# Kernel tuning notes

Hardware: AMD Instinct MI355X
Metric: run time of the kernel (lower is better)

## Reference

```python
import jax, jax.numpy as jnp
import numpy as np

GOP = 4


def conv3x3(x, w, b):
    y = jax.lax.conv_general_dilated(x, w, (1, 1), 'SAME',
                                     dimension_numbers=('NCHW', 'OIHW', 'NCHW'))
    return y + b[None, :, None, None]


def resize_bilinear(x, oh, ow):
    # F.interpolate(mode='bilinear', align_corners=False), no antialias
    N, C, H, W = x.shape
    ys = (jnp.arange(oh, dtype=x.dtype) + 0.5) * (H / oh) - 0.5
    xs = (jnp.arange(ow, dtype=x.dtype) + 0.5) * (W / ow) - 0.5
    y0 = jnp.floor(ys); x0 = jnp.floor(xs)
    ty = (ys - y0)[:, None]; tx = (xs - x0)[None, :]
    y0i = jnp.clip(y0, 0, H - 1).astype(jnp.int32)
    y1i = jnp.clip(y0 + 1, 0, H - 1).astype(jnp.int32)
    x0i = jnp.clip(x0, 0, W - 1).astype(jnp.int32)
    x1i = jnp.clip(x0 + 1, 0, W - 1).astype(jnp.int32)
    r00 = x[:, :, y0i][:, :, :, x0i]; r01 = x[:, :, y0i][:, :, :, x1i]
    r10 = x[:, :, y1i][:, :, :, x0i]; r11 = x[:, :, y1i][:, :, :, x1i]
    top = r00 * (1 - tx) + r01 * tx
    bot = r10 * (1 - tx) + r11 * tx
    return top * (1 - ty) + bot * ty


def deform_sample_1x1(feat, off):
    # torchvision deform_conv2d with 1x1 kernel: bilinear gather at
    # (h + dy, w + dx), zero outside; offset channels are (dy, dx).
    N, C, H, W = feat.shape
    dy, dx = off[:, 0], off[:, 1]                       # [N,H,W]
    gy = jnp.arange(H, dtype=feat.dtype)[:, None] + dy  # [N,H,W]
    gx = jnp.arange(W, dtype=feat.dtype)[None, :] + dx
    y0 = jnp.floor(gy); x0 = jnp.floor(gx)
    ty = (gy - y0)[:, None]; tx = (gx - x0)[:, None]    # [N,1,H,W]

    def corner(yi, xi):
        valid = (yi >= 0) & (yi < H) & (xi >= 0) & (xi < W)
        yc = jnp.clip(yi, 0, H - 1).astype(jnp.int32)
        xc = jnp.clip(xi, 0, W - 1).astype(jnp.int32)
        v = jax.vmap(lambda f, y, x: f[:, y, x])(feat, yc, xc)  # [N,C,H,W]
        return v * valid[:, None].astype(feat.dtype)

    return (corner(y0, x0) * (1 - ty) * (1 - tx)
            + corner(y0, x0 + 1) * (1 - ty) * tx
            + corner(y0 + 1, x0) * ty * (1 - tx)
            + corner(y0 + 1, x0 + 1) * ty * tx)


def setup_inputs() -> dict:
    key = jax.random.key(0)
    ks = jax.random.split(key, 20)
    dim = 256
    f32 = jnp.float32

    def p(k, shape, s=0.05):
        return jax.random.normal(k, shape, dtype=f32) * s

    return {
        'imgs': jax.random.normal(ks[0], (2, 16, 3, 224, 224), dtype=f32),
        'i_features': jax.random.normal(ks[1], (8, dim, 56, 56), dtype=f32),
        'p_motions': jax.random.normal(ks[2], (2, 12, 2, 112, 112), dtype=f32),
        'dw': p(ks[3], (dim, dim)), 'db': p(ks[4], (dim,)),
        'mw1': p(ks[5], (dim, dim, 3, 3)), 'mb1': p(ks[6], (dim,)),
        'mw2': p(ks[7], (dim, dim, 3, 3)), 'mb2': p(ks[8], (dim,)),
        'mw3': p(ks[9], (dim, dim, 3, 3)), 'mb3': p(ks[10], (dim,)),
        'ew1': p(ks[11], (dim, 2, 3, 3)), 'eb1': p(ks[12], (dim,)),
        'ew2': p(ks[13], (dim, dim, 3, 3)), 'eb2': p(ks[14], (dim,)),
        'ew3': p(ks[15], (dim, dim, 3, 3)), 'eb3': p(ks[16], (dim,)),
        'ew4': p(ks[17], (dim, dim, 3, 3)), 'eb4': p(ks[18], (dim,)),
    }


def reference(imgs, i_features, p_motions, dw, db, mw1, mb1, mw2, mb2, mw3, mb3,
              ew1, eb1, ew2, eb2, ew3, eb3, ew4, eb4):
    B = imgs.shape[0]
    num_gop = imgs.shape[1] // GOP
    h, w = i_features.shape[-2], i_features.shape[-1]
    scale = h / imgs.shape[-1]  # static python float
    Tp = p_motions.shape[1]
    k = Tp // num_gop

    # flatten motions over (b t), resize to feature res, rescale magnitudes
    pm = p_motions.reshape(B * Tp, 2, p_motions.shape[-2], p_motions.shape[-1])
    pm = resize_bilinear(pm, h, w) * scale              # [(b n k), 2, h, w]

    emb = jax.nn.relu(conv3x3(pm, ew1, eb1))
    emb = jax.nn.relu(conv3x3(emb, ew2, eb2))
    emb = jax.nn.relu(conv3x3(emb, ew3, eb3))
    emb = jax.nn.relu(conv3x3(emb, ew4, eb4))

    # i_features expanded to one copy per P-frame: (b n) -> (b n k)
    feat = jnp.repeat(i_features, k, axis=0)
    sampled = deform_sample_1x1(feat, pm)
    pf = jnp.einsum('nchw,oc->nohw', sampled, dw) + db[None, :, None, None]

    pf = jax.nn.relu(conv3x3(pf, mw1, mb1))
    pf = jax.nn.relu(conv3x3(pf, mw2, mb2))
    pf = jax.nn.relu(conv3x3(pf, mw3, mb3))
    p2d = pf + emb                                      # [(b n k), c, h, w]

    # adaptive_avg_pool2d(1) + flatten(3)
    pooled = p2d.reshape(B, num_gop, k, -1, h, w).mean(axis=(-2, -1))  # [b,n,k,c]
    return pooled, p2d
```

## Files before the change

kernel.cpp:

```cpp
#include <hip/hip_runtime.h>

#define NPIX 3136
#define NN   24
#define CDIM 256

typedef __attribute__((ext_vector_type(8))) short short8v;
typedef __attribute__((ext_vector_type(4))) float float4v;

typedef __attribute__((address_space(1))) const void gvoid;
typedef __attribute__((address_space(3))) void lvoid;
static __device__ __forceinline__ void async_copy16(const void* g, void* l) {
    __builtin_amdgcn_global_load_lds((gvoid*)g, (lvoid*)l, 16, 0, 0);
}

static __device__ __forceinline__ unsigned short f2b(float f) {
    unsigned int u = __float_as_uint(f);
    u = (u + 0x7FFFu + ((u >> 16) & 1u)) >> 16;
    return (unsigned short)u;
}
static __device__ __forceinline__ float b2f(unsigned short h) {
    return __uint_as_float(((unsigned int)h) << 16);
}

__global__ __launch_bounds__(256) void resize_pm_kernel(
    const float* __restrict__ pmo, float* __restrict__ pm)
{
    int idx = blockIdx.x * 256 + threadIdx.x;
    if (idx >= NN * 2 * NPIX) return;
    int x = idx % 56, y = (idx / 56) % 56, nc = idx / NPIX;
    const float* src = pmo + (size_t)nc * 112 * 112 + (size_t)(2 * y) * 112 + 2 * x;
    pm[idx] = (src[0] + src[1] + src[112] + src[113]) * 0.0625f;
}

__global__ __launch_bounds__(256) void pack_all_kernel(
    const float* __restrict__ s0, const float* __restrict__ s1,
    const float* __restrict__ s2, const float* __restrict__ s3,
    const float* __restrict__ s4, const float* __restrict__ s5,
    const float* __restrict__ sdw, unsigned short* __restrict__ dstbase)
{
    int bx = blockIdx.x;
    if (bx < 6 * 2304) {
        int wi = bx / 2304;
        int d = (bx % 2304) * 256 + threadIdx.x;
        const float* w = (wi == 0) ? s0 : (wi == 1) ? s1 : (wi == 2) ? s2
                       : (wi == 3) ? s3 : (wi == 4) ? s4 : s5;
        int j = d & 7;
        int lane = (d >> 3) & 63;
        int g = (d >> 9) & 3;
        int e = d >> 11;
        int tap = e % 9;
        int f = e / 9;
        int ch = f & 7, cb = f >> 3;
        int co = cb * 64 + g * 16 + (lane & 15);
        int ci = ch * 32 + (lane >> 4) * 8 + j;
        dstbase[(size_t)wi * 589824 + d] = f2b(w[((size_t)co * 256 + ci) * 9 + tap]);
    } else {
        int d = (bx - 6 * 2304) * 256 + threadIdx.x;
        int j = d & 7;
        int lane = (d >> 3) & 63;
        int g = (d >> 9) & 3;
        int ch = (d >> 11) & 7;
        int cb = d >> 14;
        int co = cb * 64 + g * 16 + (lane & 15);
        int ci = ch * 32 + (lane >> 4) * 8 + j;
        dstbase[(size_t)6 * 589824 + d] = f2b(sdw[(size_t)co * 256 + ci]);
    }
}

__global__ __launch_bounds__(256) void ew1_kernel(
    const float* __restrict__ pm, const float* __restrict__ w,
    const float* __restrict__ b, unsigned short* __restrict__ out)
{
    __shared__ float sT[8][18];
    __shared__ float sW1[256 * 19];
    int n = blockIdx.y;
    int pixbase = blockIdx.x * 8;
    int t = threadIdx.x;
    if (t < 144) {
        int p = t / 18, j = t % 18;
        int ci = j / 9, tap = j % 9;
        int pix = pixbase + p;
        int y = pix / 56, x = pix % 56;
        int yy = y + tap / 3 - 1, xx = x + tap % 3 - 1;
        float v = 0.f;
        if ((unsigned)yy < 56u && (unsigned)xx < 56u)
            v = pm[((size_t)n * 2 + ci) * NPIX + yy * 56 + xx];
        sT[p][j] = v;
    }
    for (int idx = t; idx < 4608; idx += 256) {
        int co = idx / 18, j = idx % 18;
        sW1[co * 19 + j] = w[idx];
    }
    __syncthreads();
    int co = t;
    float bias = b[co];
#pragma unroll
    for (int p = 0; p < 8; p++) {
        float acc = bias;
#pragma unroll
        for (int j = 0; j < 18; j++) acc += sT[p][j] * sW1[co * 19 + j];
        acc = fmaxf(acc, 0.f);
        out[((size_t)n * NPIX + pixbase + p) * 256 + co] = f2b(acc);
    }
}

template <int TAPS, bool RELU, bool HASB, bool FUSE>
__global__ __launch_bounds__(256, 2) void conv_mfma(
    const unsigned short* __restrict__ in,
    const unsigned short* __restrict__ wp,
    const float* __restrict__ bias,
    unsigned short* __restrict__ out,
    const unsigned short* __restrict__ inB,
    const unsigned short* __restrict__ wpB,
    const float* __restrict__ biasB,
    unsigned short* __restrict__ outB,
    int zsplit,
    const unsigned short* __restrict__ emb,
    float* __restrict__ dout)
{
    constexpr int W_ITERS = TAPS * 4;
    constexpr int SIN_SHORTS = (TAPS == 9) ? 10 * 58 * 32 : 448 * 32;

    __shared__ unsigned short sIn[SIN_SHORTS];
    __shared__ unsigned short sW[W_ITERS * 512];

    const int r0 = blockIdx.x * 8;
    if (r0 >= 56) return;
    const int tid = threadIdx.x;
    const int lane = tid & 63;
    const int wv = tid >> 6;
    const int col = lane & 15;
    const int quad = lane >> 4;
    const int cb = blockIdx.y;

    int n = blockIdx.z;
    const unsigned short* inP = in;
    const unsigned short* wpP = wp;
    const float* biasP = bias;
    unsigned short* outP = out;
    if (n >= zsplit) {
        n -= zsplit;
        inP = inB; wpP = wpB; biasP = biasB; outP = outB;
    }

    const unsigned short* inN = inP + (size_t)n * NPIX * 256;
    const unsigned short* wcb = wpP + (size_t)cb * 8 * W_ITERS * 512;

    int rowoff[7];
#pragma unroll
    for (int nj = 0; nj < 7; nj++) {
        int pxl = wv * 112 + nj * 16 + col;
        if (TAPS == 9) {
            int yl = pxl / 56;
            rowoff[nj] = yl * 58 + (pxl - yl * 56);
        } else {
            rowoff[nj] = pxl;
        }
    }
    const int qoff = quad * 8;
    const int laneSrc = (lane >> 2) * 256 + (lane & 3) * 8;

    if (TAPS == 9) {
        for (int i = tid * 8; i < SIN_SHORTS; i += 2048)
            *(int4*)(sIn + i) = (int4){0, 0, 0, 0};
    }

    float4v acc[4][7];
#pragma unroll
    for (int mi = 0; mi < 4; mi++)
#pragma unroll
        for (int nj = 0; nj < 7; nj++) acc[mi][nj] = (float4v){0.f, 0.f, 0.f, 0.f};

    for (int ch = 0; ch < 8; ch++) {
        const int c0 = ch * 32;
        __syncthreads();
        const unsigned short* wchunk = wcb + (size_t)ch * W_ITERS * 512;
#pragma unroll
        for (int it = wv; it < W_ITERS; it += 4)
            async_copy16(wchunk + it * 512 + lane * 8, sW + it * 512);
        if (TAPS == 9) {
#pragma unroll
            for (int ry = 0; ry < 10; ry++) {
                int k = (wv - ry) & 3;
                int gy = r0 + ry - 1;
                if ((unsigned)gy < 56u && (k < 3 || lane < 32))
                    async_copy16(inN + (size_t)gy * 14336 + k * 4096 + c0 + laneSrc,
                                 sIn + ry * 1856 + 32 + k * 512);
            }
        } else {
#pragma unroll
            for (int k = 0; k < 7; k++) {
                int it = wv + k * 4;
                async_copy16(inN + (size_t)r0 * 14336 + it * 4096 + c0 + laneSrc,
                             sIn + it * 512);
            }
        }
        __syncthreads();
#pragma unroll
        for (int tap = 0; tap < TAPS; tap++) {
            const int coff = (TAPS == 9) ? ((tap / 3) * 58 + (tap % 3)) * 32 : 0;
            short8v a[4], b[7];
#pragma unroll
            for (int mi = 0; mi < 4; mi++)
                a[mi] = *(const short8v*)(sW + ((tap * 4 + mi) * 64 + lane) * 8);
#pragma unroll
            for (int nj = 0; nj < 7; nj++)
                b[nj] = *(const short8v*)(sIn + rowoff[nj] * 32 + coff + qoff);
#pragma unroll
            for (int mi = 0; mi < 4; mi++)
#pragma unroll
                for (int nj = 0; nj < 7; nj++)
                    acc[mi][nj] = __builtin_amdgcn_mfma_f32_16x16x32_bf16(
                        a[mi], b[nj], acc[mi][nj], 0, 0, 0);
        }
    }

    if (!FUSE) {
        unsigned short* outT = outP + ((size_t)n * NPIX + r0 * 56 + wv * 112) * 256 + cb * 64;
#pragma unroll
        for (int mi = 0; mi < 4; mi++) {
            float4v bv = (float4v){0.f, 0.f, 0.f, 0.f};
            if (HASB) bv = *(const float4v*)(biasP + cb * 64 + mi * 16 + quad * 4);
#pragma unroll
            for (int nj = 0; nj < 7; nj++) {
                float v0 = acc[mi][nj][0] + bv[0];
                float v1 = acc[mi][nj][1] + bv[1];
                float v2 = acc[mi][nj][2] + bv[2];
                float v3 = acc[mi][nj][3] + bv[3];
                if (RELU) {
                    v0 = fmaxf(v0, 0.f); v1 = fmaxf(v1, 0.f);
                    v2 = fmaxf(v2, 0.f); v3 = fmaxf(v3, 0.f);
                }
                uint2 pk;
                pk.x = (unsigned)f2b(v0) | ((unsigned)f2b(v1) << 16);
                pk.y = (unsigned)f2b(v2) | ((unsigned)f2b(v3) << 16);
                *(uint2*)(outT + ((size_t)(nj * 16 + col)) * 256 + mi * 16 + quad * 4) = pk;
            }
        }
    } else {
        const int pixBase = r0 * 56 + wv * 112;
        float* p2d = dout + 6144 + (size_t)n * CDIM * NPIX;
        float sums[4][4];
#pragma unroll
        for (int mi = 0; mi < 4; mi++)
#pragma unroll
            for (int q = 0; q < 4; q++) sums[mi][q] = 0.f;
#pragma unroll
        for (int mi = 0; mi < 4; mi++) {
            float4v bv = *(const float4v*)(biasP + cb * 64 + mi * 16 + quad * 4);
            const int co0 = cb * 64 + mi * 16 + quad * 4;
#pragma unroll
            for (int nj = 0; nj < 7; nj++) {
                int pix = pixBase + nj * 16 + col;
                uint2 e = *(const uint2*)(emb + ((size_t)n * NPIX + pix) * 256 + co0);
                float v0 = fmaxf(acc[mi][nj][0] + bv[0], 0.f) + b2f((unsigned short)(e.x & 0xFFFF));
                float v1 = fmaxf(acc[mi][nj][1] + bv[1], 0.f) + b2f((unsigned short)(e.x >> 16));
                float v2 = fmaxf(acc[mi][nj][2] + bv[2], 0.f) + b2f((unsigned short)(e.y & 0xFFFF));
                float v3 = fmaxf(acc[mi][nj][3] + bv[3], 0.f) + b2f((unsigned short)(e.y >> 16));
                p2d[(size_t)(co0 + 0) * NPIX + pix] = v0;
                p2d[(size_t)(co0 + 1) * NPIX + pix] = v1;
                p2d[(size_t)(co0 + 2) * NPIX + pix] = v2;
                p2d[(size_t)(co0 + 3) * NPIX + pix] = v3;
                sums[mi][0] += v0; sums[mi][1] += v1;
                sums[mi][2] += v2; sums[mi][3] += v3;
            }
        }
#pragma unroll
        for (int mi = 0; mi < 4; mi++)
#pragma unroll
            for (int q = 0; q < 4; q++) {
                float s = sums[mi][q];
                s += __shfl_down(s, 8, 16);
                s += __shfl_down(s, 4, 16);
                s += __shfl_down(s, 2, 16);
                s += __shfl_down(s, 1, 16);
                if (col == 0)
                    atomicAdd(dout + n * CDIM + cb * 64 + mi * 16 + quad * 4 + q,
                              s * (1.f / 3136.f));
            }
    }
}

__global__ __launch_bounds__(256) void transpose_fI(
    const float* __restrict__ feat, unsigned short* __restrict__ dst)
{
    __shared__ float s[64][65];
    int fi = blockIdx.z;
    int p0 = blockIdx.x * 64;
    int c0 = blockIdx.y * 64;
    int t = threadIdx.x;
    int pl = t & 63, cq = t >> 6;
#pragma unroll
    for (int i = 0; i < 16; i++) {
        int c = cq + i * 4;
        s[pl][c] = feat[((size_t)fi * 256 + c0 + c) * NPIX + p0 + pl];
    }
    __syncthreads();
    int cl = t & 63, pq = t >> 6;
#pragma unroll
    for (int i = 0; i < 16; i++) {
        int p = pq + i * 4;
        dst[((size_t)fi * NPIX + p0 + p) * 256 + c0 + cl] = f2b(s[p][cl]);
    }
}

__global__ __launch_bounds__(256) void deform_kernel(
    const unsigned short* __restrict__ Z,
    const float* __restrict__ pm,
    const float* __restrict__ db,
    unsigned short* __restrict__ out)
{
    int n = blockIdx.y;
    int t = threadIdx.x;
    int pix = blockIdx.x * 8 + (t >> 5);
    int g = t & 31;
    int fi = n / 3;
    int y = pix / 56, x = pix % 56;
    float dy = pm[((size_t)n * 2 + 0) * NPIX + pix];
    float dx = pm[((size_t)n * 2 + 1) * NPIX + pix];
    float gy = (float)y + dy, gx = (float)x + dx;
    float y0f = floorf(gy), x0f = floorf(gx);
    float ty = gy - y0f, tx = gx - x0f;
    int y0 = (int)y0f, x0 = (int)x0f, y1 = y0 + 1, x1 = x0 + 1;
    bool vy0 = (unsigned)y0 < 56u, vy1 = (unsigned)y1 < 56u;
    bool vx0 = (unsigned)x0 < 56u, vx1 = (unsigned)x1 < 56u;
    float w00 = (1.f - ty) * (1.f - tx) * (vy0 && vx0 ? 1.f : 0.f);
    float w01 = (1.f - ty) * tx * (vy0 && vx1 ? 1.f : 0.f);
    float w10 = ty * (1.f - tx) * (vy1 && vx0 ? 1.f : 0.f);
    float w11 = ty * tx * (vy1 && vx1 ? 1.f : 0.f);
    int y0c = vy0 ? y0 : 0, y1c = vy1 ? y1 : 0;
    int x0c = vx0 ? x0 : 0, x1c = vx1 ? x1 : 0;
    const unsigned short* Zf = Z + (size_t)fi * NPIX * 256 + g * 8;
    const unsigned short* p00 = Zf + (size_t)(y0c * 56 + x0c) * 256;
    const unsigned short* p01 = Zf + (size_t)(y0c * 56 + x1c) * 256;
    const unsigned short* p10 = Zf + (size_t)(y1c * 56 + x0c) * 256;
    const unsigned short* p11 = Zf + (size_t)(y1c * 56 + x1c) * 256;
    unsigned short r[8];
#pragma unroll
    for (int j = 0; j < 8; j++) {
        float v = b2f(p00[j]) * w00 + b2f(p01[j]) * w01 +
                  b2f(p10[j]) * w10 + b2f(p11[j]) * w11;
        v += db[g * 8 + j];
        r[j] = f2b(v);
    }
    *(int4*)(out + ((size_t)n * NPIX + pix) * 256 + g * 8) = *(int4*)r;
}

extern "C" void kernel_launch(void* const* d_in, const int* in_sizes, int n_in,
                              void* d_out, int out_size, void* d_ws, size_t ws_size,
                              hipStream_t stream)
{
    const float* i_features = (const float*)d_in[1];
    const float* p_motions  = (const float*)d_in[2];
    const float* dw  = (const float*)d_in[3];
    const float* db  = (const float*)d_in[4];
    const float* mw1 = (const float*)d_in[5];
    const float* mb1 = (const float*)d_in[6];
    const float* mw2 = (const float*)d_in[7];
    const float* mb2 = (const float*)d_in[8];
    const float* mw3 = (const float*)d_in[9];
    const float* mb3 = (const float*)d_in[10];
    const float* ew1 = (const float*)d_in[11];
    const float* eb1 = (const float*)d_in[12];
    const float* ew2 = (const float*)d_in[13];
    const float* eb2 = (const float*)d_in[14];
    const float* ew3 = (const float*)d_in[15];
    const float* eb3 = (const float*)d_in[16];
    const float* ew4 = (const float*)d_in[17];
    const float* eb4 = (const float*)d_in[18];
    float* out = (float*)d_out;

    const size_t SZ_PM  = 602112;
    const size_t SZ_WPK = 7208960;
    const size_t SZ_ACT = 38535168;
    char* p = (char*)d_ws;
    float* pm = (float*)p;            p += SZ_PM;
    unsigned short* wpk = (unsigned short*)p;
    unsigned short* wpE2 = wpk + 0 * 589824;
    unsigned short* wpE3 = wpk + 1 * 589824;
    unsigned short* wpE4 = wpk + 2 * 589824;
    unsigned short* wpM1 = wpk + 3 * 589824;
    unsigned short* wpM2 = wpk + 4 * 589824;
    unsigned short* wpM3 = wpk + 5 * 589824;
    unsigned short* wpDW = wpk + 6 * 589824;
    p += SZ_WPK;
    unsigned short* bufA = (unsigned short*)p; p += SZ_ACT;
    unsigned short* bufB = (unsigned short*)p; p += SZ_ACT;
    unsigned short* bufC = (unsigned short*)p; p += SZ_ACT;
    unsigned short* bufD = (unsigned short*)p;

    const bool paired = ws_size >= SZ_PM + SZ_WPK + 4 * SZ_ACT;

    hipMemsetAsync(out, 0, 6144 * sizeof(float), stream);

    resize_pm_kernel<<<(NN * 2 * NPIX + 255) / 256, 256, 0, stream>>>(p_motions, pm);
    pack_all_kernel<<<6 * 2304 + 256, 256, 0, stream>>>(
        ew2, ew3, ew4, mw1, mw2, mw3, dw, wpk);

    dim3 cg24(8, 4, NN), cg48(8, 4, 2 * NN), cg8(8, 4, 8);

    if (paired) {
        ew1_kernel<<<dim3(392, NN), 256, 0, stream>>>(pm, ew1, eb1, bufA);
        conv_mfma<9, true, true, false><<<cg24, 256, 0, stream>>>(
            bufA, wpE2, eb2, bufB,  bufA, wpE2, eb2, bufB, NN, nullptr, nullptr);
        unsigned short* fI = bufA;
        unsigned short* Zb = bufA + (size_t)8 * NPIX * 256;
        transpose_fI<<<dim3(49, 4, 8), 256, 0, stream>>>(i_features, fI);
        conv_mfma<1, false, false, false><<<cg8, 256, 0, stream>>>(
            fI, wpDW, nullptr, Zb,  fI, wpDW, nullptr, Zb, NN, nullptr, nullptr);
        deform_kernel<<<dim3(392, NN), 256, 0, stream>>>(Zb, pm, db, bufC);
        conv_mfma<9, true, true, false><<<cg48, 256, 0, stream>>>(
            bufB, wpE3, eb3, bufA,  bufC, wpM1, mb1, bufD, NN, nullptr, nullptr);
        conv_mfma<9, true, true, false><<<cg48, 256, 0, stream>>>(
            bufA, wpE4, eb4, bufB,  bufD, wpM2, mb2, bufC, NN, nullptr, nullptr);
        conv_mfma<9, true, true, true><<<cg24, 256, 0, stream>>>(
            bufC, wpM3, mb3, nullptr,  bufC, wpM3, mb3, nullptr, NN, bufB, out);
    } else {
        ew1_kernel<<<dim3(392, NN), 256, 0, stream>>>(pm, ew1, eb1, bufA);
        conv_mfma<9, true, true, false><<<cg24, 256, 0, stream>>>(
            bufA, wpE2, eb2, bufB,  bufA, wpE2, eb2, bufB, NN, nullptr, nullptr);
        conv_mfma<9, true, true, false><<<cg24, 256, 0, stream>>>(
            bufB, wpE3, eb3, bufA,  bufB, wpE3, eb3, bufA, NN, nullptr, nullptr);
        conv_mfma<9, true, true, false><<<cg24, 256, 0, stream>>>(
            bufA, wpE4, eb4, bufC,  bufA, wpE4, eb4, bufC, NN, nullptr, nullptr);
        transpose_fI<<<dim3(49, 4, 8), 256, 0, stream>>>(i_features, bufA);
        conv_mfma<1, false, false, false><<<cg8, 256, 0, stream>>>(
            bufA, wpDW, nullptr, bufB,  bufA, wpDW, nullptr, bufB, NN, nullptr, nullptr);
        deform_kernel<<<dim3(392, NN), 256, 0, stream>>>(bufB, pm, db, bufA);
        conv_mfma<9, true, true, false><<<cg24, 256, 0, stream>>>(
            bufA, wpM1, mb1, bufB,  bufA, wpM1, mb1, bufB, NN, nullptr, nullptr);
        conv_mfma<9, true, true, false><<<cg24, 256, 0, stream>>>(
            bufB, wpM2, mb2, bufA,  bufB, wpM2, mb2, bufA, NN, nullptr, nullptr);
        conv_mfma<9, true, true, true><<<cg24, 256, 0, stream>>>(
            bufA, wpM3, mb3, nullptr,  bufA, wpM3, mb3, nullptr, NN, bufC, out);
    }
}
```

Before: 692.3 us.

## Double-buffer LDS weight and input tiles in the MFMA conv kernel

Doubles the shared-memory buffers for weights and input tiles so the async global-to-LDS copies for the next 32-channel chunk are issued before computing the current chunk. This removes one barrier per chunk and is meant to hide global load latency behind the MFMA work. The cost is double the LDS footprint (roughly 148KB for the 3x3 variant), which likely drops occupancy from two blocks per CU to one. That could offset the gain from overlap.

```diff
diff --git a/kernel.cpp b/kernel.cpp
--- a/kernel.cpp
+++ b/kernel.cpp
@@ -120,9 +120,10 @@
 {
     constexpr int W_ITERS = TAPS * 4;
     constexpr int SIN_SHORTS = (TAPS == 9) ? 10 * 58 * 32 : 448 * 32;
-
-    __shared__ unsigned short sIn[SIN_SHORTS];
-    __shared__ unsigned short sW[W_ITERS * 512];
+    constexpr int SW_SHORTS = W_ITERS * 512;
+
+    __shared__ unsigned short sIn[2 * SIN_SHORTS];
+    __shared__ unsigned short sW[2 * SW_SHORTS];
 
     const int r0 = blockIdx.x * 8;
     if (r0 >= 56) return;
@@ -160,24 +161,16 @@
     const int qoff = quad * 8;
     const int laneSrc = (lane >> 2) * 256 + (lane & 3) * 8;
 
-    if (TAPS == 9) {
-        for (int i = tid * 8; i < SIN_SHORTS; i += 2048)
-            *(int4*)(sIn + i) = (int4){0, 0, 0, 0};
-    }
-
-    float4v acc[4][7];
-#pragma unroll
-    for (int mi = 0; mi < 4; mi++)
-#pragma unroll
-        for (int nj = 0; nj < 7; nj++) acc[mi][nj] = (float4v){0.f, 0.f, 0.f, 0.f};
-
-    for (int ch = 0; ch < 8; ch++) {
+    auto stageW = [&](int ch, int half) {
+        const unsigned short* wchunk = wcb + (size_t)ch * W_ITERS * 512;
+        unsigned short* dst = sW + half * SW_SHORTS;
+#pragma unroll
+        for (int it = wv; it < W_ITERS; it += 4)
+            async_copy16(wchunk + it * 512 + lane * 8, dst + it * 512);
+    };
+    auto stageI = [&](int ch, int half) {
         const int c0 = ch * 32;
-        __syncthreads();
-        const unsigned short* wchunk = wcb + (size_t)ch * W_ITERS * 512;
-#pragma unroll
-        for (int it = wv; it < W_ITERS; it += 4)
-            async_copy16(wchunk + it * 512 + lane * 8, sW + it * 512);
+        unsigned short* dst = sIn + half * SIN_SHORTS;
         if (TAPS == 9) {
 #pragma unroll
             for (int ry = 0; ry < 10; ry++) {
@@ -185,27 +178,51 @@
                 int gy = r0 + ry - 1;
                 if ((unsigned)gy < 56u && (k < 3 || lane < 32))
                     async_copy16(inN + (size_t)gy * 14336 + k * 4096 + c0 + laneSrc,
-                                 sIn + ry * 1856 + 32 + k * 512);
+                                 dst + ry * 1856 + 32 + k * 512);
             }
         } else {
 #pragma unroll
             for (int k = 0; k < 7; k++) {
                 int it = wv + k * 4;
                 async_copy16(inN + (size_t)r0 * 14336 + it * 4096 + c0 + laneSrc,
-                             sIn + it * 512);
+                             dst + it * 512);
             }
         }
+    };
+
+    if (TAPS == 9) {
+        for (int i = tid * 8; i < 2 * SIN_SHORTS; i += 2048)
+            *(int4*)(sIn + i) = (int4){0, 0, 0, 0};
         __syncthreads();
+    }
+
+    float4v acc[4][7];
+#pragma unroll
+    for (int mi = 0; mi < 4; mi++)
+#pragma unroll
+        for (int nj = 0; nj < 7; nj++) acc[mi][nj] = (float4v){0.f, 0.f, 0.f, 0.f};
+
+    stageW(0, 0);
+    stageI(0, 0);
+
+    for (int ch = 0; ch < 8; ch++) {
+        __syncthreads();
+        if (ch < 7) {
+            stageW(ch + 1, (ch + 1) & 1);
+            stageI(ch + 1, (ch + 1) & 1);
+        }
+        const int wOff = (ch & 1) * SW_SHORTS;
+        const int iOff = (ch & 1) * SIN_SHORTS;
 #pragma unroll
         for (int tap = 0; tap < TAPS; tap++) {
             const int coff = (TAPS == 9) ? ((tap / 3) * 58 + (tap % 3)) * 32 : 0;
             short8v a[4], b[7];
 #pragma unroll
             for (int mi = 0; mi < 4; mi++)
-                a[mi] = *(const short8v*)(sW + ((tap * 4 + mi) * 64 + lane) * 8);
+                a[mi] = *(const short8v*)(sW + wOff + ((tap * 4 + mi) * 64 + lane) * 8);
 #pragma unroll
             for (int nj = 0; nj < 7; nj++)
-                b[nj] = *(const short8v*)(sIn + rowoff[nj] * 32 + coff + qoff);
+                b[nj] = *(const short8v*)(sIn + iOff + rowoff[nj] * 32 + coff + qoff);
 #pragma unroll
             for (int mi = 0; mi < 4; mi++)
 #pragma unroll
```

Result: slower. 822.1 us (+18.8%).

## Add 512-thread conv kernel computing 128 output channels per block

Applied to the files above, without the earlier changes.

Adds a new conv8_mfma kernel in which each 512-thread block computes 128 output channels (two wave groups of 64) over 8 rows, instead of 64 channels with 256 threads. The weight packing layout is changed to match for all weights except the final fused conv, which keeps the old kernel and layout. The intent is to reuse each staged input tile across twice as many output channels, halving input LDS staging traffic per MFMA. In exchange the grid has half as many blocks and each block uses more LDS and registers, which may lower occupancy.

```diff
diff --git a/kernel.cpp b/kernel.cpp
--- a/kernel.cpp
+++ b/kernel.cpp
@@ -46,22 +46,33 @@
                        : (wi == 3) ? s3 : (wi == 4) ? s4 : s5;
         int j = d & 7;
         int lane = (d >> 3) & 63;
-        int g = (d >> 9) & 3;
-        int e = d >> 11;
-        int tap = e % 9;
-        int f = e / 9;
-        int ch = f & 7, cb = f >> 3;
-        int co = cb * 64 + g * 16 + (lane & 15);
-        int ci = ch * 32 + (lane >> 4) * 8 + j;
+        int co, ci, tap;
+        if (wi == 5) {
+            int g = (d >> 9) & 3;
+            int e = d >> 11;
+            tap = e % 9;
+            int f = e / 9;
+            int ch = f & 7, cb = f >> 3;
+            co = cb * 64 + g * 16 + (lane & 15);
+            ci = ch * 32 + (lane >> 4) * 8 + j;
+        } else {
+            int mi = (d >> 9) & 7;
+            int e = d >> 12;
+            tap = e % 9;
+            int f = e / 9;
+            int ch = f & 7, cb = f >> 3;
+            co = cb * 128 + mi * 16 + (lane & 15);
+            ci = ch * 32 + (lane >> 4) * 8 + j;
+        }
         dstbase[(size_t)wi * 589824 + d] = f2b(w[((size_t)co * 256 + ci) * 9 + tap]);
     } else {
         int d = (bx - 6 * 2304) * 256 + threadIdx.x;
         int j = d & 7;
         int lane = (d >> 3) & 63;
-        int g = (d >> 9) & 3;
-        int ch = (d >> 11) & 7;
-        int cb = d >> 14;
-        int co = cb * 64 + g * 16 + (lane & 15);
+        int mi = (d >> 9) & 7;
+        int e = d >> 12;
+        int ch = e & 7, cb = e >> 3;
+        int co = cb * 128 + mi * 16 + (lane & 15);
         int ci = ch * 32 + (lane >> 4) * 8 + j;
         dstbase[(size_t)6 * 589824 + d] = f2b(sdw[(size_t)co * 256 + ci]);
     }
@@ -101,6 +112,154 @@
         for (int j = 0; j < 18; j++) acc += sT[p][j] * sW1[co * 19 + j];
         acc = fmaxf(acc, 0.f);
         out[((size_t)n * NPIX + pixbase + p) * 256 + co] = f2b(acc);
+    }
+}
+
+template <int TAPS, bool RELU, bool HASB>
+__global__ __launch_bounds__(512, 2) void conv8_mfma(
+    const unsigned short* __restrict__ in,
+    const unsigned short* __restrict__ wp,
+    const float* __restrict__ bias,
+    unsigned short* __restrict__ out,
+    const unsigned short* __restrict__ inB,
+    const unsigned short* __restrict__ wpB,
+    const float* __restrict__ biasB,
+    unsigned short* __restrict__ outB,
+    int zsplit)
+{
+    constexpr int W_ITERS = TAPS * 8;
+    constexpr int SIN_SHORTS = (TAPS == 9) ? 10 * 58 * 32 : 448 * 32;
+
+    __shared__ unsigned short sIn[2 * SIN_SHORTS];
+    __shared__ unsigned short sW[W_ITERS * 512];
+
+    const int r0 = blockIdx.x * 8;
+    if (r0 >= 56) return;
+    const int tid = threadIdx.x;
+    const int lane = tid & 63;
+    const int wv = tid >> 6;
+    const int mih = wv >> 2;
+    const int wpx = wv & 3;
+    const int col = lane & 15;
+    const int quad = lane >> 4;
+    const int cb = blockIdx.y;
+
+    int n = blockIdx.z;
+    const unsigned short* inP = in;
+    const unsigned short* wpP = wp;
+    const float* biasP = bias;
+    unsigned short* outP = out;
+    if (n >= zsplit) {
+        n -= zsplit;
+        inP = inB; wpP = wpB; biasP = biasB; outP = outB;
+    }
+
+    const unsigned short* inN = inP + (size_t)n * NPIX * 256;
+    const unsigned short* wcb = wpP + (size_t)cb * 8 * W_ITERS * 512;
+
+    int rowoff[7];
+#pragma unroll
+    for (int nj = 0; nj < 7; nj++) {
+        int pxl = wpx * 112 + nj * 16 + col;
+        if (TAPS == 9) {
+            int yl = pxl / 56;
+            rowoff[nj] = yl * 58 + (pxl - yl * 56);
+        } else {
+            rowoff[nj] = pxl;
+        }
+    }
+    const int qoff = quad * 8;
+    const int laneSrc = (lane >> 2) * 256 + (lane & 3) * 8;
+
+    auto stageW = [&](int ch) {
+        const unsigned short* wchunk = wcb + (size_t)ch * W_ITERS * 512;
+#pragma unroll
+        for (int it = wv; it < W_ITERS; it += 8)
+            async_copy16(wchunk + it * 512 + lane * 8, sW + it * 512);
+    };
+    auto stageI = [&](int ch, int half) {
+        const int c0 = ch * 32;
+        unsigned short* dst = sIn + half * SIN_SHORTS;
+        if (TAPS == 9) {
+#pragma unroll
+            for (int s = wv; s < 40; s += 8) {
+                int ry = s >> 2, k = s & 3;
+                int gy = r0 + ry - 1;
+                if ((unsigned)gy < 56u && (k < 3 || lane < 32))
+                    async_copy16(inN + (size_t)gy * 14336 + k * 4096 + c0 + laneSrc,
+                                 dst + ry * 1856 + 32 + k * 512);
+            }
+        } else {
+#pragma unroll
+            for (int s = wv; s < 28; s += 8)
+                async_copy16(inN + (size_t)r0 * 14336 + s * 4096 + c0 + laneSrc,
+                             dst + s * 512);
+        }
+    };
+
+    if (TAPS == 9) {
+        for (int i = tid * 8; i < 2 * SIN_SHORTS; i += 512 * 8)
+            *(int4*)(sIn + i) = (int4){0, 0, 0, 0};
+        __syncthreads();
+    }
+
+    float4v acc[4][7];
+#pragma unroll
+    for (int mi = 0; mi < 4; mi++)
+#pragma unroll
+        for (int nj = 0; nj < 7; nj++) acc[mi][nj] = (float4v){0.f, 0.f, 0.f, 0.f};
+
+    stageW(0);
+    stageI(0, 0);
+
+    for (int ch = 0; ch < 8; ch++) {
+        __syncthreads();
+        if (ch < 7) stageI(ch + 1, (ch + 1) & 1);
+        const int iOff = (ch & 1) * SIN_SHORTS;
+#pragma unroll
+        for (int tap = 0; tap < TAPS; tap++) {
+            const int coff = (TAPS == 9) ? ((tap / 3) * 58 + (tap % 3)) * 32 : 0;
+            short8v a[4], b[7];
+#pragma unroll
+            for (int mi = 0; mi < 4; mi++)
+                a[mi] = *(const short8v*)(sW + ((tap * 8 + mih * 4 + mi) * 64 + lane) * 8);
+#pragma unroll
+            for (int nj = 0; nj < 7; nj++)
+                b[nj] = *(const short8v*)(sIn + iOff + rowoff[nj] * 32 + coff + qoff);
+#pragma unroll
+            for (int mi = 0; mi < 4; mi++)
+#pragma unroll
+                for (int nj = 0; nj < 7; nj++)
+                    acc[mi][nj] = __builtin_amdgcn_mfma_f32_16x16x32_bf16(
+                        a[mi], b[nj], acc[mi][nj], 0, 0, 0);
+        }
+        if (ch < 7) {
+            __syncthreads();
+            stageW(ch + 1);
+        }
+    }
+
+    unsigned short* outT = outP + ((size_t)n * NPIX + r0 * 56 + wpx * 112) * 256
+                         + cb * 128 + mih * 64;
+#pragma unroll
+    for (int mi = 0; mi < 4; mi++) {
+        float4v bv = (float4v){0.f, 0.f, 0.f, 0.f};
+        if (HASB) bv = *(const float4v*)(biasP + cb * 128 + mih * 64 + mi * 16 + quad * 4);
+#pragma unroll
+        for (int nj = 0; nj < 7; nj++) {
+            float v0 = acc[mi][nj][0] + bv[0];
+            float v1 = acc[mi][nj][1] + bv[1];
+            float v2 = acc[mi][nj][2] + bv[2];
+            float v3 = acc[mi][nj][3] + bv[3];
+            if (RELU) {
+                v0 = fmaxf(v0, 0.f); v1 = fmaxf(v1, 0.f);
+                v2 = fmaxf(v2, 0.f); v3 = fmaxf(v3, 0.f);
+            }
+            uint2 pk;
+            pk.x = (unsigned)f2b(v0) | ((unsigned)f2b(v1) << 16);
+            pk.y = (unsigned)f2b(v2) | ((unsigned)f2b(v3) << 16);
+            *(uint2*)(outT + ((size_t)(nj * 16 + col)) * 256 + mi * 16 + quad * 4) = pk;
+        }
     }
 }
 
@@ -397,41 +556,42 @@
     pack_all_kernel<<<6 * 2304 + 256, 256, 0, stream>>>(
         ew2, ew3, ew4, mw1, mw2, mw3, dw, wpk);
 
-    dim3 cg24(8, 4, NN), cg48(8, 4, 2 * NN), cg8(8, 4, 8);
+    dim3 cg24(8, 2, NN), cg48(8, 2, 2 * NN), cg8(8, 2, 8);
+    dim3 cgF(8, 4, NN);
 
     if (paired) {
         ew1_kernel<<<dim3(392, NN), 256, 0, stream>>>(pm, ew1, eb1, bufA);
-        conv_mfma<9, true, true, false><<<cg24, 256, 0, stream>>>(
-            bufA, wpE2, eb2, bufB,  bufA, wpE2, eb2, bufB, NN, nullptr, nullptr);
+        conv8_mfma<9, true, true><<<cg24, 512, 0, stream>>>(
+            bufA, wpE2, eb2, bufB,  bufA, wpE2, eb2, bufB, NN);
         unsigned short* fI = bufA;
         unsigned short* Zb = bufA + (size_t)8 * NPIX * 256;
         transpose_fI<<<dim3(49, 4, 8), 256, 0, stream>>>(i_features, fI);
-        conv_mfma<1, false, false, false><<<cg8, 256, 0, stream>>>(
-            fI, wpDW, nullptr, Zb,  fI, wpDW, nullptr, Zb, NN, nullptr, nullptr);
+        conv8_mfma<1, false, false><<<cg8, 512, 0, stream>>>(
+            fI, wpDW, nullptr, Zb,  fI, wpDW, nullptr, Zb, NN);
         deform_kernel<<<dim3(392, NN), 256, 0, stream>>>(Zb, pm, db, bufC);
-        conv_mfma<9, true, true, false><<<cg48, 256, 0, stream>>>(
-            bufB, wpE3, eb3, bufA,  bufC, wpM1, mb1, bufD, NN, nullptr, nullptr);
-        conv_mfma<9, true, true, false><<<cg48, 256, 0, stream>>>(
-            bufA, wpE4, eb4, bufB,  bufD, wpM2, mb2, bufC, NN, nullptr, nullptr);
-        conv_mfma<9, true, true, true><<<cg24, 256, 0, stream>>>(
+        conv8_mfma<9, true, true><<<cg48, 512, 0, stream>>>(
+            bufB, wpE3, eb3, bufA,  bufC, wpM1, mb1, bufD, NN);
+        conv8_mfma<9, true, true><<<cg48, 512, 0, stream>>>(
+            bufA, wpE4, eb4, bufB,  bufD, wpM2, mb2, bufC, NN);
+        conv_mfma<9, true, true, true><<<cgF, 256, 0, stream>>>(
             bufC, wpM3, mb3, nullptr,  bufC, wpM3, mb3, nullptr, NN, bufB, out);
     } else {
         ew1_kernel<<<dim3(392, NN), 256, 0, stream>>>(pm, ew1, eb1, bufA);
-        conv_mfma<9, true, true, false><<<cg24, 256, 0, stream>>>(
-            bufA, wpE2, eb2, bufB,  bufA, wpE2, eb2, bufB, NN, nullptr, nullptr);
-        conv_mfma<9, true, true, false><<<cg24, 256, 0, stream>>>(
-            bufB, wpE3, eb3, bufA,  bufB, wpE3, eb3, bufA, NN, nullptr, nullptr);
-        conv_mfma<9, true, true, false><<<cg24, 256, 0, stream>>>(
-            bufA, wpE4, eb4, bufC,  bufA, wpE4, eb4, bufC, NN, nullptr, nullptr);
+        conv8_mfma<9, true, true><<<cg24, 512, 0, stream>>>(
+            bufA, wpE2, eb2, bufB,  bufA, wpE2, eb2, bufB, NN);
+        conv8_mfma<9, true, true><<<cg24, 512, 0, stream>>>(
+            bufB, wpE3, eb3, bufA,  bufB, wpE3, eb3, bufA, NN);
+        conv8_mfma<9, true, true><<<cg24, 512, 0, stream>>>(
+            bufA, wpE4, eb4, bufC,  bufA, wpE4, eb4, bufC, NN);
         transpose_fI<<<dim3(49, 4, 8), 256, 0, stream>>>(i_features, bufA);
-        conv_mfma<1, false, false, false><<<cg8, 256, 0, stream>>>(
-            bufA, wpDW, nullptr, bufB,  bufA, wpDW, nullptr, bufB, NN, nullptr, nullptr);
+        conv8_mfma<1, false, false><<<cg8, 512, 0, stream>>>(
+            bufA, wpDW, nullptr, bufB,  bufA, wpDW, nullptr, bufB, NN);
         deform_kernel<<<dim3(392, NN), 256, 0, stream>>>(bufB, pm, db, bufA);
-        conv_mfma<9, true, true, false><<<cg24, 256, 0, stream>>>(
-            bufA, wpM1, mb1, bufB,  bufA, wpM1, mb1, bufB, NN, nullptr, nullptr);
-        conv_mfma<9, true, true, false><<<cg24, 256, 0, stream>>>(
-            bufB, wpM2, mb2, bufA,  bufB, wpM2, mb2, bufA, NN, nullptr, nullptr);
-        conv_mfma<9, true, true, true><<<cg24, 256, 0, stream>>>(
+        conv8_mfma<9, true, true><<<cg24, 512, 0, stream>>>(
+            bufA, wpM1, mb1, bufB,  bufA, wpM1, mb1, bufB, NN);
+        conv8_mfma<9, true, true><<<cg24, 512, 0, stream>>>(
+            bufB, wpM2, mb2, bufA,  bufB, wpM2, mb2, bufA, NN);
+        conv_mfma<9, true, true, true><<<cgF, 256, 0, stream>>>(
             bufA, wpM3, mb3, nullptr,  bufA, wpM3, mb3, nullptr, NN, bufC, out);
     }
 }
```

New measurement: 751.6 us. +8.6%, slower.

## Merge ew1 with fI transpose and pair conv2 with 1x1 projection in one launch

Applied to the files above, without the earlier changes.

Folds the i_features transpose into the ew1 kernel as extra blocks, and runs the first embedding 3x3 conv together with the 1x1 deform projection in a single heterogeneous launch via a templated conv_pair wrapper. The goal is fewer kernel launches and better GPU fill, since the small transpose and 1x1 conv grids used to run alone. To avoid aliasing, the fI/Zb scratch moves to bufD. In exchange, shared memory is sized for the 3x3 case in every variant, and the ew1 kernel now declares a large transpose tile it mostly leaves unused, which may reduce occupancy.

```diff
diff --git a/kernel.cpp b/kernel.cpp
--- a/kernel.cpp
+++ b/kernel.cpp
@@ -67,81 +67,87 @@
     }
 }
 
-__global__ __launch_bounds__(256) void ew1_kernel(
+__global__ __launch_bounds__(256) void ew1_fI_kernel(
     const float* __restrict__ pm, const float* __restrict__ w,
-    const float* __restrict__ b, unsigned short* __restrict__ out)
+    const float* __restrict__ b, unsigned short* __restrict__ outEw,
+    const float* __restrict__ feat, unsigned short* __restrict__ outFI,
+    int ewBlocks)
 {
     __shared__ float sT[8][18];
     __shared__ float sW1[256 * 19];
-    int n = blockIdx.y;
-    int pixbase = blockIdx.x * 8;
+    __shared__ float sTr[64][65];
+    int bx = blockIdx.x;
     int t = threadIdx.x;
-    if (t < 144) {
-        int p = t / 18, j = t % 18;
-        int ci = j / 9, tap = j % 9;
-        int pix = pixbase + p;
-        int y = pix / 56, x = pix % 56;
-        int yy = y + tap / 3 - 1, xx = x + tap % 3 - 1;
-        float v = 0.f;
-        if ((unsigned)yy < 56u && (unsigned)xx < 56u)
-            v = pm[((size_t)n * 2 + ci) * NPIX + yy * 56 + xx];
-        sT[p][j] = v;
-    }
-    for (int idx = t; idx < 4608; idx += 256) {
-        int co = idx / 18, j = idx % 18;
-        sW1[co * 19 + j] = w[idx];
-    }
-    __syncthreads();
-    int co = t;
-    float bias = b[co];
-#pragma unroll
-    for (int p = 0; p < 8; p++) {
-        float acc = bias;
-#pragma unroll
-        for (int j = 0; j < 18; j++) acc += sT[p][j] * sW1[co * 19 + j];
-        acc = fmaxf(acc, 0.f);
-        out[((size_t)n * NPIX + pixbase + p) * 256 + co] = f2b(acc);
+    if (bx < ewBlocks) {
+        int n = bx / 392;
+        int pixbase = (bx % 392) * 8;
+        if (t < 144) {
+            int p = t / 18, j = t % 18;
+            int ci = j / 9, tap = j % 9;
+            int pix = pixbase + p;
+            int y = pix / 56, x = pix % 56;
+            int yy = y + tap / 3 - 1, xx = x + tap % 3 - 1;
+            float v = 0.f;
+            if ((unsigned)yy < 56u && (unsigned)xx < 56u)
+                v = pm[((size_t)n * 2 + ci) * NPIX + yy * 56 + xx];
+            sT[p][j] = v;
+        }
+        for (int idx = t; idx < 4608; idx += 256) {
+            int co = idx / 18, j = idx % 18;
+            sW1[co * 19 + j] = w[idx];
+        }
+        __syncthreads();
+        int co = t;
+        float bias = b[co];
+#pragma unroll
+        for (int p = 0; p < 8; p++) {
+            float acc = bias;
+#pragma unroll
+            for (int j = 0; j < 18; j++) acc += sT[p][j] * sW1[co * 19 + j];
+            acc = fmaxf(acc, 0.f);
+            outEw[((size_t)n * NPIX + pixbase + p) * 256 + co] = f2b(acc);
+        }
+    } else {
+        int b2 = bx - ewBlocks;
+        int fi = b2 / 196;
+        int rem = b2 % 196;
+        int c0 = (rem / 49) * 64;
+        int p0 = (rem % 49) * 64;
+        int pl = t & 63, cq = t >> 6;
+#pragma unroll
+        for (int i = 0; i < 16; i++) {
+            int c = cq + i * 4;
+            sTr[pl][c] = feat[((size_t)fi * 256 + c0 + c) * NPIX + p0 + pl];
+        }
+        __syncthreads();
+        int cl = t & 63, pq = t >> 6;
+#pragma unroll
+        for (int i = 0; i < 16; i++) {
+            int p = pq + i * 4;
+            outFI[((size_t)fi * NPIX + p0 + p) * 256 + c0 + cl] = f2b(sTr[p][cl]);
+        }
     }
 }
 
 template <int TAPS, bool RELU, bool HASB, bool FUSE>
-__global__ __launch_bounds__(256, 2) void conv_mfma(
-    const unsigned short* __restrict__ in,
-    const unsigned short* __restrict__ wp,
-    const float* __restrict__ bias,
-    unsigned short* __restrict__ out,
-    const unsigned short* __restrict__ inB,
-    const unsigned short* __restrict__ wpB,
-    const float* __restrict__ biasB,
-    unsigned short* __restrict__ outB,
-    int zsplit,
+static __device__ __forceinline__ void conv_body(
+    unsigned short* sIn, unsigned short* sW,
+    const unsigned short* __restrict__ inP,
+    const unsigned short* __restrict__ wpP,
+    const float* __restrict__ biasP,
+    unsigned short* __restrict__ outP,
+    int n, int r0, int cb,
     const unsigned short* __restrict__ emb,
     float* __restrict__ dout)
 {
     constexpr int W_ITERS = TAPS * 4;
     constexpr int SIN_SHORTS = (TAPS == 9) ? 10 * 58 * 32 : 448 * 32;
 
-    __shared__ unsigned short sIn[SIN_SHORTS];
-    __shared__ unsigned short sW[W_ITERS * 512];
-
-    const int r0 = blockIdx.x * 8;
-    if (r0 >= 56) return;
     const int tid = threadIdx.x;
     const int lane = tid & 63;
     const int wv = tid >> 6;
     const int col = lane & 15;
     const int quad = lane >> 4;
-    const int cb = blockIdx.y;
-
-    int n = blockIdx.z;
-    const unsigned short* inP = in;
-    const unsigned short* wpP = wp;
-    const float* biasP = bias;
-    unsigned short* outP = out;
-    if (n >= zsplit) {
-        n -= zsplit;
-        inP = inB; wpP = wpB; biasP = biasB; outP = outB;
-    }
 
     const unsigned short* inN = inP + (size_t)n * NPIX * 256;
     const unsigned short* wcb = wpP + (size_t)cb * 8 * W_ITERS * 512;
@@ -279,6 +285,32 @@
                               s * (1.f / 3136.f));
             }
     }
+}
+
+template <int TA, bool RA, bool HA, int TB, bool RB, bool HB, bool FUSE>
+__global__ __launch_bounds__(256, 2) void conv_pair(
+    const unsigned short* __restrict__ inA,
+    const unsigned short* __restrict__ wpA,
+    const float* __restrict__ bA, unsigned short* __restrict__ oA,
+    const unsigned short* __restrict__ inB,
+    const unsigned short* __restrict__ wpB,
+    const float* __restrict__ bB, unsigned short* __restrict__ oB,
+    int zsplit,
+    const unsigned short* __restrict__ emb,
+    float* __restrict__ dout)
+{
+    __shared__ unsigned short sIn[10 * 58 * 32];
+    __shared__ unsigned short sW[36 * 512];
+
+    const int r0 = blockIdx.x * 8;
+    if (r0 >= 56) return;
+    int n = blockIdx.z;
+    if (n >= zsplit)
+        conv_body<TB, RB, HB, FUSE>(sIn, sW, inB, wpB, bB, oB,
+                                    n - zsplit, r0, blockIdx.y, emb, dout);
+    else
+        conv_body<TA, RA, HA, FUSE>(sIn, sW, inA, wpA, bA, oA,
+                                    n, r0, blockIdx.y, emb, dout);
 }
 
 __global__ __launch_bounds__(256) void transpose_fI(
@@ -397,41 +429,43 @@
     pack_all_kernel<<<6 * 2304 + 256, 256, 0, stream>>>(
         ew2, ew3, ew4, mw1, mw2, mw3, dw, wpk);
 
-    dim3 cg24(8, 4, NN), cg48(8, 4, 2 * NN), cg8(8, 4, 8);
+    const int ewBlocks = 392 * NN;
+    dim3 cg48(8, 4, 2 * NN), cgF(8, 4, NN);
 
     if (paired) {
-        ew1_kernel<<<dim3(392, NN), 256, 0, stream>>>(pm, ew1, eb1, bufA);
-        conv_mfma<9, true, true, false><<<cg24, 256, 0, stream>>>(
-            bufA, wpE2, eb2, bufB,  bufA, wpE2, eb2, bufB, NN, nullptr, nullptr);
-        unsigned short* fI = bufA;
-        unsigned short* Zb = bufA + (size_t)8 * NPIX * 256;
-        transpose_fI<<<dim3(49, 4, 8), 256, 0, stream>>>(i_features, fI);
-        conv_mfma<1, false, false, false><<<cg8, 256, 0, stream>>>(
-            fI, wpDW, nullptr, Zb,  fI, wpDW, nullptr, Zb, NN, nullptr, nullptr);
+        unsigned short* fI = bufD;
+        unsigned short* Zb = bufD + (size_t)8 * NPIX * 256;
+        ew1_fI_kernel<<<ewBlocks + 49 * 4 * 8, 256, 0, stream>>>(
+            pm, ew1, eb1, bufA, i_features, fI, ewBlocks);
+        conv_pair<9, true, true, 1, false, false, false>
+            <<<dim3(8, 4, NN + 8), 256, 0, stream>>>(
+            bufA, wpE2, eb2, bufB,  fI, wpDW, nullptr, Zb, NN, nullptr, nullptr);
         deform_kernel<<<dim3(392, NN), 256, 0, stream>>>(Zb, pm, db, bufC);
-        conv_mfma<9, true, true, false><<<cg48, 256, 0, stream>>>(
+        conv_pair<9, true, true, 9, true, true, false><<<cg48, 256, 0, stream>>>(
             bufB, wpE3, eb3, bufA,  bufC, wpM1, mb1, bufD, NN, nullptr, nullptr);
-        conv_mfma<9, true, true, false><<<cg48, 256, 0, stream>>>(
+        conv_pair<9, true, true, 9, true, true, false><<<cg48, 256, 0, stream>>>(
             bufA, wpE4, eb4, bufB,  bufD, wpM2, mb2, bufC, NN, nullptr, nullptr);
-        conv_mfma<9, true, true, true><<<cg24, 256, 0, stream>>>(
+        conv_pair<9, true, true, 9, true, true, true><<<cgF, 256, 0, stream>>>(
             bufC, wpM3, mb3, nullptr,  bufC, wpM3, mb3, nullptr, NN, bufB, out);
     } else {
-        ew1_kernel<<<dim3(392, NN), 256, 0, stream>>>(pm, ew1, eb1, bufA);
-        conv_mfma<9, true, true, false><<<cg24, 256, 0, stream>>>(
+        ew1_fI_kernel<<<ewBlocks, 256, 0, stream>>>(
+            pm, ew1, eb1, bufA, nullptr, nullptr, ewBlocks);
+        conv_pair<9, true, true, 9, true, true, false><<<cgF, 256, 0, stream>>>(
             bufA, wpE2, eb2, bufB,  bufA, wpE2, eb2, bufB, NN, nullptr, nullptr);
-        conv_mfma<9, true, true, false><<<cg24, 256, 0, stream>>>(
+        conv_pair<9, true, true, 9, true, true, false><<<cgF, 256, 0, stream>>>(
             bufB, wpE3, eb3, bufA,  bufB, wpE3, eb3, bufA, NN, nullptr, nullptr);
-        conv_mfma<9, true, true, false><<<cg24, 256, 0, stream>>>(
+        conv_pair<9, true, true, 9, true, true, false><<<cgF, 256, 0, stream>>>(
             bufA, wpE4, eb4, bufC,  bufA, wpE4, eb4, bufC, NN, nullptr, nullptr);
         transpose_fI<<<dim3(49, 4, 8), 256, 0, stream>>>(i_features, bufA);
-        conv_mfma<1, false, false, false><<<cg8, 256, 0, stream>>>(
-            bufA, wpDW, nullptr, bufB,  bufA, wpDW, nullptr, bufB, NN, nullptr, nullptr);
+        conv_pair<1, false, false, 1, false, false, false>
+            <<<dim3(8, 4, 8), 256, 0, stream>>>(
+            bufA, wpDW, nullptr, bufB,  bufA, wpDW, nullptr, bufB, 8, nullptr, nullptr);
         deform_kernel<<<dim3(392, NN), 256, 0, stream>>>(bufB, pm, db, bufA);
-        conv_mfma<9, true, true, false><<<cg24, 256, 0, stream>>>(
+        conv_pair<9, true, true, 9, true, true, false><<<cgF, 256, 0, stream>>>(
             bufA, wpM1, mb1, bufB,  bufA, wpM1, mb1, bufB, NN, nullptr, nullptr);
-        conv_mfma<9, true, true, false><<<cg24, 256, 0, stream>>>(
+        conv_pair<9, true, true, 9, true, true, false><<<cgF, 256, 0, stream>>>(
             bufB, wpM2, mb2, bufA,  bufB, wpM2, mb2, bufA, NN, nullptr, nullptr);
-        conv_mfma<9, true, true, true><<<cg24, 256, 0, stream>>>(
+        conv_pair<9, true, true, 9, true, true, true><<<cgF, 256, 0, stream>>>(
             bufA, wpM3, mb3, nullptr,  bufA, wpM3, mb3, nullptr, NN, bufC, out);
     }
 }
```

After: 676.8 us. 2.2% less time.
